# Kernel tuning notes

Hardware: AMD Instinct MI355X
Metric: run time of the kernel (lower is better)

Reference implementation:

```python
import jax, jax.numpy as jnp
import numpy as np
from jax.scipy.special import logsumexp

B, T, D, K, H, A, EH = 256, 4096, 3, 2, 2, 5, 8


def setup_inputs() -> dict:
    key = jax.random.key(0)
    ks = jax.random.split(key, 14)
    p = lambda k, shape: jax.random.normal(k, shape, jnp.float32) * 0.1
    return {
        "x": jax.random.normal(ks[0], (B, T, D), jnp.float32),
        "Q_seq": jax.random.normal(ks[1], (B, T, A, 2), jnp.float32),
        "log_pi": p(ks[2], (K,)),
        "log_A": p(ks[3], (K, K)),
        "fc1_w": p(ks[4], (EH, D)),
        "fc1_b": p(ks[5], (EH,)),
        "fc2_w": p(ks[6], (K, EH)),
        "fc2_b": p(ks[7], (K,)),
        "w_ih": p(ks[8], (3 * H, D)),
        "w_hh": p(ks[9], (3 * H, H)),
        "b_ih": p(ks[10], (3 * H,)),
        "b_hh": p(ks[11], (3 * H,)),
        "Wg": p(ks[12], (K, H, A)),
        "by": p(ks[13], (K, 2)),
    }


def reference(x, Q_seq, log_pi, log_A, fc1_w, fc1_b, fc2_w, fc2_b,
              w_ih, w_hh, b_ih, b_hh, Wg, by):
    Bn, Tn, _ = x.shape
    Hn = w_hh.shape[1]

    # ---- GRU (torch semantics: r,z,n gate order) ----
    def gru_step(h, xt):
        gi = xt @ w_ih.T + b_ih            # [B,3H]
        gh = h @ w_hh.T + b_hh
        ir, iz, inn = jnp.split(gi, 3, axis=-1)
        hr, hz, hn = jnp.split(gh, 3, axis=-1)
        r = jax.nn.sigmoid(ir + hr)
        z = jax.nn.sigmoid(iz + hz)
        n = jnp.tanh(inn + r * hn)
        h_new = (1.0 - z) * n + z * h
        return h_new, h_new

    xs = jnp.swapaxes(x, 0, 1)             # [T,B,D]
    _, hs = jax.lax.scan(gru_step, jnp.zeros((Bn, Hn), x.dtype), xs)
    h = jnp.swapaxes(hs, 0, 1)             # [B,T,H]

    # ---- Phase emitter ----
    e = jax.nn.log_softmax(jnp.tanh(x @ fc1_w.T + fc1_b) @ fc2_w.T + fc2_b, axis=-1)  # [B,T,K]

    # ---- HMM forward-backward ----
    lpi = jax.nn.log_softmax(log_pi)
    lA = jax.nn.log_softmax(log_A, axis=1)
    eT = jnp.swapaxes(e, 0, 1)             # [T,B,K]

    a0 = lpi + eT[0]
    def astep(a, et):
        an = logsumexp(a[:, :, None] + lA[None], axis=1) + et
        return an, an
    _, arest = jax.lax.scan(astep, a0, eT[1:])
    alpha = jnp.concatenate([a0[None], arest], axis=0)   # [T,B,K]

    bN = jnp.zeros_like(a0)
    def bstep(b, et1):
        bt = logsumexp(b[:, None, :] + lA[None] + et1[:, None, :], axis=2)
        return bt, bt
    _, brest = jax.lax.scan(bstep, bN, eT[1:], reverse=True)
    beta = jnp.concatenate([brest, bN[None]], axis=0)    # [T,B,K]

    lg = alpha + beta
    lg = lg - logsumexp(lg, axis=-1, keepdims=True)
    log_gamma = jnp.swapaxes(lg, 0, 1)     # [B,T,K]
    gamma = jnp.exp(log_gamma)

    # ---- Mixture-of-agents gating ----
    Wh = jnp.einsum('bth,kha->btka', h, Wg)
    gk = jax.nn.softmax(Wh, axis=-1)
    g = jnp.einsum('btk,btka->bta', gamma, gk)
    V = jnp.einsum('bta,btay->bty', g, Q_seq) + jnp.einsum('btk,kc->btc', gamma, by)
    pi_log = jax.nn.log_softmax(V, axis=-1)
    return pi_log, g, log_gamma
```

## Files before the change

### kernel.cpp

```cpp
#include <hip/hip_runtime.h>
#include <hip/hip_fp16.h>
#include <math.h>

constexpr int Bn = 256;
constexpr int Tn = 4096;
constexpr int BT = Bn * Tn;

constexpr int CG  = 32;
constexpr int CAc = 64;
constexpr int CBc = 64;
constexpr int NGRU = (Tn / CG)  * (Bn / 64);
constexpr int NALP = (Tn / CAc) * (Bn / 64);
constexpr int NBET = (Tn / CBc) * (Bn / 64);

struct __align__(8) h4 { __half2 x, y; };

typedef float  v2f __attribute__((ext_vector_type(2)));

__device__ __forceinline__ float2 f2(float a, float b){ return make_float2(a,b); }
__device__ __forceinline__ float2 f2s(float a){ return make_float2(a,a); }
__device__ __forceinline__ float2 f2mul(float2 a, float2 b){ return f2(a.x*b.x, a.y*b.y); }
__device__ __forceinline__ float2 f2fma(float2 a, float2 b, float2 c){
  return f2(fmaf(a.x,b.x,c.x), fmaf(a.y,b.y,c.y)); }

__device__ __forceinline__ __half2 h2c(float v){ return __float2half2_rn(v); }

__device__ __forceinline__ __half2 sig2h(__half2 x) {
  __half2 x2 = __hmul2(x, x);
  __half2 p = __hfma2(x2, h2c(2.0833333e-3f), h2c(-2.0833333e-2f));
  p = __hfma2(x2, p, h2c(0.25f));
  return __hfma2(x, p, h2c(0.5f));
}
__device__ __forceinline__ __half2 tanh2h(__half2 x) {
  __half2 x2 = __hmul2(x, x);
  __half2 num = __hfma2(x2, __hadd2(x2, h2c(105.f)), h2c(945.f));
  __half2 den = __hfma2(x2, __hfma2(x2, h2c(15.f), h2c(420.f)), h2c(945.f));
  float2 df = __half22float2(den);
  __half2 rd = __floats2half2_rn(__builtin_amdgcn_rcpf(df.x),
                                 __builtin_amdgcn_rcpf(df.y));
  return __hmul2(__hmul2(x, num), rd);
}

__global__ __launch_bounds__(256) void k1_pre(
    const float* __restrict__ x,
    const float* __restrict__ fc1_w, const float* __restrict__ fc1_b,
    const float* __restrict__ fc2_w, const float* __restrict__ fc2_b,
    const float* __restrict__ w_ih,  const float* __restrict__ b_ih,
    const float* __restrict__ b_hh,
    h4* __restrict__ grz, __half2* __restrict__ gn, __half2* __restrict__ E)
{
  __shared__ h4      Lg[16][17];
  __shared__ __half2 Ln[16][17];
  __shared__ __half2 LE[16][17];
  int tid = threadIdx.x;
  int btile = blockIdx.x >> 8;
  int ttile = blockIdx.x & 255;

  {
    int bl = tid >> 4, tl = tid & 15;
    int b = btile * 16 + bl, t = ttile * 16 + tl;
    const float* xp = x + ((size_t)b * Tn + t) * 3;
    float x0 = xp[0], x1 = xp[1], x2 = xp[2];

    float gr0 = fmaf(x2, w_ih[2],  fmaf(x1, w_ih[1],  fmaf(x0, w_ih[0],  b_ih[0] + b_hh[0])));
    float gr1 = fmaf(x2, w_ih[5],  fmaf(x1, w_ih[4],  fmaf(x0, w_ih[3],  b_ih[1] + b_hh[1])));
    float gz0 = fmaf(x2, w_ih[8],  fmaf(x1, w_ih[7],  fmaf(x0, w_ih[6],  b_ih[2] + b_hh[2])));
    float gz1 = fmaf(x2, w_ih[11], fmaf(x1, w_ih[10], fmaf(x0, w_ih[9],  b_ih[3] + b_hh[3])));
    float gn0 = fmaf(x2, w_ih[14], fmaf(x1, w_ih[13], fmaf(x0, w_ih[12], b_ih[4])));
    float gn1 = fmaf(x2, w_ih[17], fmaf(x1, w_ih[16], fmaf(x0, w_ih[15], b_ih[5])));

    float zk0 = fc2_b[0], zk1 = fc2_b[1];
#pragma unroll
    for (int u = 0; u < 8; ++u) {
      float a = fmaf(x2, fc1_w[u*3+2], fmaf(x1, fc1_w[u*3+1], fmaf(x0, fc1_w[u*3+0], fc1_b[u])));
      float e2 = __expf(2.0f * a);
      float th = 1.0f - 2.0f * __builtin_amdgcn_rcpf(1.0f + e2);
      zk0 = fmaf(th, fc2_w[u], zk0);
      zk1 = fmaf(th, fc2_w[8 + u], zk1);
    }
    float m = fmaxf(zk0, zk1);
    h4 g; g.x = __float22half2_rn(f2(gr0, gr1)); g.y = __float22half2_rn(f2(gz0, gz1));
    Lg[tl][bl] = g;
    Ln[tl][bl] = __float22half2_rn(f2(gn0, gn1));
    LE[tl][bl] = __float22half2_rn(f2(__expf(zk0 - m), __expf(zk1 - m)));
  }
  __syncthreads();
  {
    int tl = tid >> 4, bl = tid & 15;
    int b = btile * 16 + bl, t = ttile * 16 + tl;
    size_t o = (size_t)t * Bn + b;
    grz[o] = Lg[tl][bl];
    gn[o]  = Ln[tl][bl];
    E[o]   = LE[tl][bl];
  }
}

#define GRU_LOAD(BG, BN_, S0) \
  { _Pragma("unroll") for (int i = 0; i < 8; ++i) { \
      BG[i] = gp[(size_t)((S0) + i) * Bn]; BN_[i] = np[(size_t)((S0) + i) * Bn]; } }

#define GRU_GROUP(BG, BN_, S0, ST) \
  { _Pragma("unroll") for (int i = 0; i < 8; ++i) { \
      __half2 gA = BG[i].x, gB = BG[i].y, gN = BN_[i]; \
      __half2 h00 = __low2half2(hh), h11 = __high2half2(hh); \
      __half2 pr = __hfma2(h00, Wr0h, __hfma2(h11, Wr1h, gA)); \
      __half2 pz = __hfma2(h00, Wz0h, __hfma2(h11, Wz1h, gB)); \
      __half2 hn = __hfma2(h00, Wn0h, __hfma2(h11, Wn1h, Bnh)); \
      __half2 r = sig2h(pr), z = sig2h(pz); \
      __half2 n = tanh2h(__hfma2(r, hn, gN)); \
      hh = __hfma2(z, __hsub2(hh, n), n); \
      if (ST) hp[(size_t)((S0) + i) * Bn] = hh; \
  } }

#define ALP_LOAD(BUF, TB) \
  { _Pragma("unroll") for (int i = 0; i < 16; ++i) { BUF[i] = Ep[(size_t)((TB) + i) * Bn]; } }

#define ALP_GROUP(BUF, TB, ST, SK) \
  { _Pragma("unroll") for (int i = 0; i < 16; ++i) { \
      float2 e2 = __half22float2(BUF[i]); \
      if (!((SK) && i == 0)) { \
        av = f2mul(f2fma(f2s(av.y), A1v, f2mul(f2s(av.x), A0v)), e2); } \
      if (ST) ap[(size_t)((TB) + i) * Bn] = __float22half2_rn(av); \
      if (i == 7 || i == 15) { \
        float rs = __builtin_amdgcn_rcpf(av.x + av.y); av.x *= rs; av.y *= rs; } \
  } }

#define BET_LOAD(BUF, TB, CL) \
  { _Pragma("unroll") for (int i = 0; i < 16; ++i) { \
      int li = (TB) + 1 - i; if ((CL) && i == 0) li = Tn - 1; \
      BUF[i] = Ep[(size_t)li * Bn]; } }

#define BET_GROUP(BUF, TB, ST, SK) \
  { _Pragma("unroll") for (int i = 0; i < 16; ++i) { \
      float2 e2 = __half22float2(BUF[i]); \
      if (!((SK) && i == 0)) { \
        float2 f = f2mul(e2, bv); \
        bv = f2fma(f2s(f.y), AB1, f2mul(f2s(f.x), AB0)); } \
      if (ST) bp[(size_t)((TB) - i) * Bn] = __float22half2_rn(bv); \
      if (i == 7 || i == 15) { \
        float rs = __builtin_amdgcn_rcpf(bv.x + bv.y); bv.x *= rs; bv.y *= rs; } \
  } }

__global__ __launch_bounds__(64) void k2_scan(
    const h4* __restrict__ grz, const __half2* __restrict__ gn,
    const __half2* __restrict__ E,
    __half2* __restrict__ h, __half2* __restrict__ alpha, __half2* __restrict__ beta,
    const float* __restrict__ w_hh, const float* __restrict__ b_hh,
    const float* __restrict__ log_pi, const float* __restrict__ log_A)
{
  int blk = blockIdx.x;
  int lane = threadIdx.x;

  if (blk < NGRU) {
    int c = blk >> 2;
    int b = ((blk & 3) << 6) + lane;
    int t0 = c * CG;
    int tstart = (c >= 2) ? (t0 - 64) : 0;
    int ng = (c == 0) ? 4 : ((c == 1) ? 8 : 12);
    int wg = (c == 0) ? 0 : ((c == 1) ? 4 : 8);
    const h4*      gp = grz + (size_t)tstart * Bn + b;
    const __half2* np = gn  + (size_t)tstart * Bn + b;
    __half2*       hp = h   + (size_t)tstart * Bn + b;

    __half2 Wr0h = __floats2half2_rn(w_hh[0], w_hh[2]);
    __half2 Wr1h = __floats2half2_rn(w_hh[1], w_hh[3]);
    __half2 Wz0h = __floats2half2_rn(w_hh[4], w_hh[6]);
    __half2 Wz1h = __floats2half2_rn(w_hh[5], w_hh[7]);
    __half2 Wn0h = __floats2half2_rn(w_hh[8], w_hh[10]);
    __half2 Wn1h = __floats2half2_rn(w_hh[9], w_hh[11]);
    __half2 Bnh  = __floats2half2_rn(b_hh[4], b_hh[5]);

    __half2 hh = h2c(0.f);
    h4 AG[8], BG[8];
    __half2 AN[8], BN[8];
    GRU_LOAD(AG, AN, 0);
    GRU_LOAD(BG, BN, 8);
    for (int g = 0; g < ng; g += 2) {
      { bool st = g >= wg; GRU_GROUP(AG, AN, g * 8, st); }
      if (g + 2 < ng) GRU_LOAD(AG, AN, (g + 2) * 8);
      { bool st = (g + 1) >= wg; GRU_GROUP(BG, BN, (g + 1) * 8, st); }
      if (g + 3 < ng) GRU_LOAD(BG, BN, (g + 3) * 8);
    }
  } else if (blk < NGRU + NALP) {
    int bk = blk - NGRU;
    int c = bk >> 2;
    int b = ((bk & 3) << 6) + lane;
    int t0 = c * CAc;
    const __half2* Ep = E + b;
    __half2* ap = alpha + b;

    float la0 = log_A[0], la1 = log_A[1], la2 = log_A[2], la3 = log_A[3];
    float m0 = fmaxf(la0, la1), m1 = fmaxf(la2, la3);
    float e00 = __expf(la0 - m0), e01 = __expf(la1 - m0);
    float e10 = __expf(la2 - m1), e11 = __expf(la3 - m1);
    float i0 = 1.0f / (e00 + e01), i1 = 1.0f / (e10 + e11);
    float2 A0v = f2(e00*i0, e01*i0), A1v = f2(e10*i1, e11*i1);

    float2 av;
    int tlo, ngroups, sg;
    bool skip0;
    if (c == 0) {
      float p0 = log_pi[0], p1 = log_pi[1];
      float mp = fmaxf(p0, p1);
      float2 E0 = __half22float2(Ep[0]);
      av = f2(__expf(p0 - mp) * E0.x, __expf(p1 - mp) * E0.y);
      tlo = 0; ngroups = 4; sg = 0; skip0 = true;
    } else {
      av = f2s(1.f);
      tlo = t0 - 32; ngroups = 6; sg = 2; skip0 = false;
    }

    __half2 EA[16], EB[16];
    ALP_LOAD(EA, tlo);
    ALP_LOAD(EB, tlo + 16);
    for (int g = 0; g < ngroups; g += 2) {
      { bool st = g >= sg; bool sk = skip0 && (g == 0);
        ALP_GROUP(EA, tlo + g * 16, st, sk); }
      if (g + 2 < ngroups) ALP_LOAD(EA, tlo + (g + 2) * 16);
      { bool st = (g + 1) >= sg;
        ALP_GROUP(EB, tlo + (g + 1) * 16, st, false); }
      if (g + 3 < ngroups) ALP_LOAD(EB, tlo + (g + 3) * 16);
    }
  } else {
    int bk = blk - NGRU - NALP;
    int c = bk >> 2;
    int b = ((bk & 3) << 6) + lane;
    int t0 = c * CBc;
    int t1 = t0 + CBc - 1;
    const __half2* Ep = E + b;
    __half2* bp = beta + b;

    float la0 = log_A[0], la1 = log_A[1], la2 = log_A[2], la3 = log_A[3];
    float m0 = fmaxf(la0, la1), m1 = fmaxf(la2, la3);
    float e00 = __expf(la0 - m0), e01 = __expf(la1 - m0);
    float e10 = __expf(la2 - m1), e11 = __expf(la3 - m1);
    float i0 = 1.0f / (e00 + e01), i1 = 1.0f / (e10 + e11);
    float2 AB0 = f2(e00*i0, e10*i1), AB1 = f2(e01*i0, e11*i1);

    float2 bv = f2s(1.f);
    int thi, ngroups, sg;
    bool skip0, cl0;
    if (t1 == Tn - 1) {
      thi = t1; ngroups = 4; sg = 0; skip0 = true; cl0 = true;
    } else {
      thi = t1 + 32; ngroups = 6; sg = 2; skip0 = false; cl0 = false;
    }

    __half2 FA[16], FB[16];
    BET_LOAD(FA, thi, cl0);
    BET_LOAD(FB, thi - 16, false);
    for (int g = 0; g < ngroups; g += 2) {
      { bool st = g >= sg; bool sk = skip0 && (g == 0);
        BET_GROUP(FA, thi - g * 16, st, sk); }
      if (g + 2 < ngroups) BET_LOAD(FA, thi - (g + 2) * 16, false);
      { bool st = (g + 1) >= sg;
        BET_GROUP(FB, thi - (g + 1) * 16, st, false); }
      if (g + 3 < ngroups) BET_LOAD(FB, thi - (g + 3) * 16, false);
    }
  }
}

__global__ __launch_bounds__(256) void k3_out(
    const __half2* __restrict__ h_, const __half2* __restrict__ a_,
    const __half2* __restrict__ b_, const float* __restrict__ Q,
    const float* __restrict__ Wg, const float* __restrict__ by,
    float* __restrict__ out_pi, float* __restrict__ out_g, float* __restrict__ out_lg)
{
  __shared__ __half2 Sh[16][17], Sa[16][17], Sb[16][17];
  int tid = threadIdx.x;
  int btile = blockIdx.x >> 8;
  int ttile = blockIdx.x & 255;
  {
    int tl = tid >> 4, bl = tid & 15;
    size_t o = (size_t)(ttile * 16 + tl) * Bn + btile * 16 + bl;
    Sh[tl][bl] = h_[o]; Sa[tl][bl] = a_[o]; Sb[tl][bl] = b_[o];
  }
  __syncthreads();
  int bl = tid >> 4, tl = tid & 15;
  int b = btile * 16 + bl, t = ttile * 16 + tl;
  size_t idx = (size_t)b * Tn + t;
  float2 hv = __half22float2(Sh[tl][bl]);
  float2 av = __half22float2(Sa[tl][bl]);
  float2 bv = __half22float2(Sb[tl][bl]);

  float p0 = av.x * bv.x, p1 = av.y * bv.y;
  float invs = 1.0f / (p0 + p1);
  float gamma0 = p0 * invs, gamma1 = p1 * invs;
  float lg0 = __logf(gamma0), lg1 = __logf(gamma1);

  float wh0[5], wh1[5];
#pragma unroll
  for (int a = 0; a < 5; ++a) {
    wh0[a] = fmaf(hv.y, Wg[5 + a],  hv.x * Wg[a]);
    wh1[a] = fmaf(hv.y, Wg[15 + a], hv.x * Wg[10 + a]);
  }
  float mx0 = wh0[0], mx1 = wh1[0];
#pragma unroll
  for (int a = 1; a < 5; ++a) { mx0 = fmaxf(mx0, wh0[a]); mx1 = fmaxf(mx1, wh1[a]); }
  float ex0[5], ex1[5];
  float s0 = 0.f, s1 = 0.f;
#pragma unroll
  for (int a = 0; a < 5; ++a) {
    ex0[a] = __expf(wh0[a] - mx0); s0 += ex0[a];
    ex1[a] = __expf(wh1[a] - mx1); s1 += ex1[a];
  }
  float r0 = 1.0f / s0, r1 = 1.0f / s1;
  float c0 = gamma0 * r0, c1 = gamma1 * r1;

  const v2f* q2 = (const v2f*)(Q + idx * 10);
  v2f qv[5];
#pragma unroll
  for (int a = 0; a < 5; ++a) qv[a] = __builtin_nontemporal_load(q2 + a);

  float V0 = fmaf(gamma1, by[2], gamma0 * by[0]);
  float V1 = fmaf(gamma1, by[3], gamma0 * by[1]);
  float ga[5];
#pragma unroll
  for (int a = 0; a < 5; ++a) {
    ga[a] = fmaf(c1, ex1[a], c0 * ex0[a]);
    V0 = fmaf(ga[a], qv[a].x, V0);
    V1 = fmaf(ga[a], qv[a].y, V1);
  }
#pragma unroll
  for (int a = 0; a < 5; ++a)
    __builtin_nontemporal_store(ga[a], out_g + idx * 5 + a);

  float mv = fmaxf(V0, V1);
  float l = mv + __logf(__expf(V0 - mv) + __expf(V1 - mv));
  v2f pi_v; pi_v.x = V0 - l; pi_v.y = V1 - l;
  v2f lg_v; lg_v.x = lg0;    lg_v.y = lg1;
  __builtin_nontemporal_store(pi_v, (v2f*)out_pi + idx);
  __builtin_nontemporal_store(lg_v, (v2f*)out_lg + idx);
}

extern "C" void kernel_launch(void* const* d_in, const int* in_sizes, int n_in,
                              void* d_out, int out_size, void* d_ws, size_t ws_size,
                              hipStream_t stream) {
  const float* x      = (const float*)d_in[0];
  const float* Q      = (const float*)d_in[1];
  const float* log_pi = (const float*)d_in[2];
  const float* log_A  = (const float*)d_in[3];
  const float* fc1_w  = (const float*)d_in[4];
  const float* fc1_b  = (const float*)d_in[5];
  const float* fc2_w  = (const float*)d_in[6];
  const float* fc2_b  = (const float*)d_in[7];
  const float* w_ih   = (const float*)d_in[8];
  const float* w_hh   = (const float*)d_in[9];
  const float* b_ih   = (const float*)d_in[10];
  const float* b_hh   = (const float*)d_in[11];
  const float* Wg     = (const float*)d_in[12];
  const float* by     = (const float*)d_in[13];

  char* ws = (char*)d_ws;
  h4*      grz   = (h4*)ws;
  __half2* gn    = (__half2*)(ws + (size_t)8  * BT);
  __half2* E     = (__half2*)(ws + (size_t)12 * BT);
  __half2* h     = (__half2*)(ws + (size_t)16 * BT);
  __half2* alpha = (__half2*)(ws + (size_t)20 * BT);
  __half2* beta  = (__half2*)(ws + (size_t)24 * BT);
  float* out = (float*)d_out;

  k1_pre<<<BT / 256, 256, 0, stream>>>(x, fc1_w, fc1_b, fc2_w, fc2_b, w_ih, b_ih, b_hh, grz, gn, E);
  k2_scan<<<NGRU + NALP + NBET, 64, 0, stream>>>(grz, gn, E, h, alpha, beta, w_hh, b_hh, log_pi, log_A);
  k3_out<<<BT / 256, 256, 0, stream>>>(h, alpha, beta, Q, Wg, by,
                                       out, out + (size_t)2 * BT, out + (size_t)7 * BT);
}
```

Measured before the change: 153.2 us.

## Fuse GRU/alpha/beta scans with output stage via shared memory per chunk

Merges the scan kernel and the output kernel into one kernel. Each 192-thread block runs the GRU, forward and backward scans in three waves over the same 32-step, 64-batch chunk, keeps h/alpha/beta in LDS, then computes the outputs directly. This removes the global write and read-back of three intermediate arrays and one kernel launch. In exchange it shrinks the alpha/beta chunks from 64 to 32 steps, so proportionally more warm-up recompute is done, and the output stage now waits behind the serial scans within each block.

```diff
diff --git a/kernel.cpp b/kernel.cpp
--- a/kernel.cpp
+++ b/kernel.cpp
@@ -6,16 +6,11 @@
 constexpr int Tn = 4096;
 constexpr int BT = Bn * Tn;
 
-constexpr int CG  = 32;
-constexpr int CAc = 64;
-constexpr int CBc = 64;
-constexpr int NGRU = (Tn / CG)  * (Bn / 64);
-constexpr int NALP = (Tn / CAc) * (Bn / 64);
-constexpr int NBET = (Tn / CBc) * (Bn / 64);
+constexpr int C   = 32;
+constexpr int NF  = (Tn / C) * (Bn / 64);
 
 struct __align__(8) h4 { __half2 x, y; };
-
-typedef float  v2f __attribute__((ext_vector_type(2)));
+typedef float v2f __attribute__((ext_vector_type(2)));
 
 __device__ __forceinline__ float2 f2(float a, float b){ return make_float2(a,b); }
 __device__ __forceinline__ float2 f2s(float a){ return make_float2(a,a); }
@@ -95,11 +90,11 @@
   }
 }
 
-#define GRU_LOAD(BG, BN_, S0) \
+#define GRU_LOAD(BG, BN_, BASE) \
   { _Pragma("unroll") for (int i = 0; i < 8; ++i) { \
-      BG[i] = gp[(size_t)((S0) + i) * Bn]; BN_[i] = np[(size_t)((S0) + i) * Bn]; } }
-
-#define GRU_GROUP(BG, BN_, S0, ST) \
+      BG[i] = gp[(size_t)((BASE) + i) * Bn]; BN_[i] = np[(size_t)((BASE) + i) * Bn]; } }
+
+#define GRU_GROUP(BG, BN_, BASE, ST) \
   { _Pragma("unroll") for (int i = 0; i < 8; ++i) { \
       __half2 gA = BG[i].x, gB = BG[i].y, gN = BN_[i]; \
       __half2 h00 = __low2half2(hh), h11 = __high2half2(hh); \
@@ -109,7 +104,7 @@
       __half2 r = sig2h(pr), z = sig2h(pz); \
       __half2 n = tanh2h(__hfma2(r, hn, gN)); \
       hh = __hfma2(z, __hsub2(hh, n), n); \
-      if (ST) hp[(size_t)((S0) + i) * Bn] = hh; \
+      if (ST) Lh[(BASE) + i - t0][lane] = hh; \
   } }
 
 #define ALP_LOAD(BUF, TB) \
@@ -120,7 +115,7 @@
       float2 e2 = __half22float2(BUF[i]); \
       if (!((SK) && i == 0)) { \
         av = f2mul(f2fma(f2s(av.y), A1v, f2mul(f2s(av.x), A0v)), e2); } \
-      if (ST) ap[(size_t)((TB) + i) * Bn] = __float22half2_rn(av); \
+      if (ST) La[(TB) + i - t0][lane] = __float22half2_rn(av); \
       if (i == 7 || i == 15) { \
         float rs = __builtin_amdgcn_rcpf(av.x + av.y); av.x *= rs; av.y *= rs; } \
   } }
@@ -136,31 +131,36 @@
       if (!((SK) && i == 0)) { \
         float2 f = f2mul(e2, bv); \
         bv = f2fma(f2s(f.y), AB1, f2mul(f2s(f.x), AB0)); } \
-      if (ST) bp[(size_t)((TB) - i) * Bn] = __float22half2_rn(bv); \
+      if (ST) Lb[(TB) - i - t0][lane] = __float22half2_rn(bv); \
       if (i == 7 || i == 15) { \
         float rs = __builtin_amdgcn_rcpf(bv.x + bv.y); bv.x *= rs; bv.y *= rs; } \
   } }
 
-__global__ __launch_bounds__(64) void k2_scan(
-    const h4* __restrict__ grz, const __half2* __restrict__ gn,
+__global__ __launch_bounds__(192) void k2_fused(
+    const h4* __restrict__ grz, const __half2* __restrict__ gnp_,
     const __half2* __restrict__ E,
-    __half2* __restrict__ h, __half2* __restrict__ alpha, __half2* __restrict__ beta,
+    const float* __restrict__ Q,
     const float* __restrict__ w_hh, const float* __restrict__ b_hh,
-    const float* __restrict__ log_pi, const float* __restrict__ log_A)
+    const float* __restrict__ log_pi, const float* __restrict__ log_A,
+    const float* __restrict__ Wg, const float* __restrict__ by,
+    float* __restrict__ out_pi, float* __restrict__ out_g, float* __restrict__ out_lg)
 {
-  int blk = blockIdx.x;
-  int lane = threadIdx.x;
-
-  if (blk < NGRU) {
-    int c = blk >> 2;
-    int b = ((blk & 3) << 6) + lane;
-    int t0 = c * CG;
-    int tstart = (c >= 2) ? (t0 - 64) : 0;
-    int ng = (c == 0) ? 4 : ((c == 1) ? 8 : 12);
-    int wg = (c == 0) ? 0 : ((c == 1) ? 4 : 8);
-    const h4*      gp = grz + (size_t)tstart * Bn + b;
-    const __half2* np = gn  + (size_t)tstart * Bn + b;
-    __half2*       hp = h   + (size_t)tstart * Bn + b;
+  __shared__ __half2 Lh[C][65], La[C][65], Lb[C][65];
+
+  int tch = blockIdx.x >> 2;
+  int bq  = blockIdx.x & 3;
+  int t0  = tch * C;
+  int wave = threadIdx.x >> 6;
+  int lane = threadIdx.x & 63;
+  int b = (bq << 6) + lane;
+
+  if (wave == 0) {
+    int warm = (tch == 0) ? 0 : 32;
+    int tstart = t0 - warm;
+    int ng = (tch == 0) ? 4 : 8;
+    int wg = warm >> 3;
+    const h4*      gp = grz  + b;
+    const __half2* np = gnp_ + b;
 
     __half2 Wr0h = __floats2half2_rn(w_hh[0], w_hh[2]);
     __half2 Wr1h = __floats2half2_rn(w_hh[1], w_hh[3]);
@@ -173,21 +173,16 @@
     __half2 hh = h2c(0.f);
     h4 AG[8], BG[8];
     __half2 AN[8], BN[8];
-    GRU_LOAD(AG, AN, 0);
-    GRU_LOAD(BG, BN, 8);
+    GRU_LOAD(AG, AN, tstart);
+    GRU_LOAD(BG, BN, tstart + 8);
     for (int g = 0; g < ng; g += 2) {
-      { bool st = g >= wg; GRU_GROUP(AG, AN, g * 8, st); }
-      if (g + 2 < ng) GRU_LOAD(AG, AN, (g + 2) * 8);
-      { bool st = (g + 1) >= wg; GRU_GROUP(BG, BN, (g + 1) * 8, st); }
-      if (g + 3 < ng) GRU_LOAD(BG, BN, (g + 3) * 8);
-    }
-  } else if (blk < NGRU + NALP) {
-    int bk = blk - NGRU;
-    int c = bk >> 2;
-    int b = ((bk & 3) << 6) + lane;
-    int t0 = c * CAc;
+      { bool st = g >= wg; GRU_GROUP(AG, AN, tstart + g * 8, st); }
+      if (g + 2 < ng) GRU_LOAD(AG, AN, tstart + (g + 2) * 8);
+      { bool st = (g + 1) >= wg; GRU_GROUP(BG, BN, tstart + (g + 1) * 8, st); }
+      if (g + 3 < ng) GRU_LOAD(BG, BN, tstart + (g + 3) * 8);
+    }
+  } else if (wave == 1) {
     const __half2* Ep = E + b;
-    __half2* ap = alpha + b;
 
     float la0 = log_A[0], la1 = log_A[1], la2 = log_A[2], la3 = log_A[3];
     float m0 = fmaxf(la0, la1), m1 = fmaxf(la2, la3);
@@ -199,15 +194,15 @@
     float2 av;
     int tlo, ngroups, sg;
     bool skip0;
-    if (c == 0) {
+    if (tch == 0) {
       float p0 = log_pi[0], p1 = log_pi[1];
       float mp = fmaxf(p0, p1);
       float2 E0 = __half22float2(Ep[0]);
       av = f2(__expf(p0 - mp) * E0.x, __expf(p1 - mp) * E0.y);
-      tlo = 0; ngroups = 4; sg = 0; skip0 = true;
+      tlo = 0; ngroups = 2; sg = 0; skip0 = true;
     } else {
       av = f2s(1.f);
-      tlo = t0 - 32; ngroups = 6; sg = 2; skip0 = false;
+      tlo = t0 - 32; ngroups = 4; sg = 2; skip0 = false;
     }
 
     __half2 EA[16], EB[16];
@@ -222,13 +217,8 @@
       if (g + 3 < ngroups) ALP_LOAD(EB, tlo + (g + 3) * 16);
     }
   } else {
-    int bk = blk - NGRU - NALP;
-    int c = bk >> 2;
-    int b = ((bk & 3) << 6) + lane;
-    int t0 = c * CBc;
-    int t1 = t0 + CBc - 1;
+    int t1 = t0 + C - 1;
     const __half2* Ep = E + b;
-    __half2* bp = beta + b;
 
     float la0 = log_A[0], la1 = log_A[1], la2 = log_A[2], la3 = log_A[3];
     float m0 = fmaxf(la0, la1), m1 = fmaxf(la2, la3);
@@ -241,9 +231,9 @@
     int thi, ngroups, sg;
     bool skip0, cl0;
     if (t1 == Tn - 1) {
-      thi = t1; ngroups = 4; sg = 0; skip0 = true; cl0 = true;
+      thi = t1; ngroups = 2; sg = 0; skip0 = true; cl0 = true;
     } else {
-      thi = t1 + 32; ngroups = 6; sg = 2; skip0 = false; cl0 = false;
+      thi = t1 + 32; ngroups = 4; sg = 2; skip0 = false; cl0 = false;
     }
 
     __half2 FA[16], FB[16];
@@ -258,79 +248,77 @@
       if (g + 3 < ngroups) BET_LOAD(FB, thi - (g + 3) * 16, false);
     }
   }
-}
-
-__global__ __launch_bounds__(256) void k3_out(
-    const __half2* __restrict__ h_, const __half2* __restrict__ a_,
-    const __half2* __restrict__ b_, const float* __restrict__ Q,
-    const float* __restrict__ Wg, const float* __restrict__ by,
-    float* __restrict__ out_pi, float* __restrict__ out_g, float* __restrict__ out_lg)
-{
-  __shared__ __half2 Sh[16][17], Sa[16][17], Sb[16][17];
+
+  __syncthreads();
+
+  float wgr[20], byv[4];
+#pragma unroll
+  for (int i = 0; i < 20; ++i) wgr[i] = Wg[i];
+#pragma unroll
+  for (int i = 0; i < 4; ++i) byv[i] = by[i];
+
   int tid = threadIdx.x;
-  int btile = blockIdx.x >> 8;
-  int ttile = blockIdx.x & 255;
-  {
-    int tl = tid >> 4, bl = tid & 15;
-    size_t o = (size_t)(ttile * 16 + tl) * Bn + btile * 16 + bl;
-    Sh[tl][bl] = h_[o]; Sa[tl][bl] = a_[o]; Sb[tl][bl] = b_[o];
+#pragma unroll
+  for (int k = 0; k < 11; ++k) {
+    int e = tid + k * 192;
+    if (e < 64 * C) {
+      int bl = e >> 5, tl = e & 31;
+      int gb = (bq << 6) + bl;
+      size_t idx = (size_t)gb * Tn + (t0 + tl);
+      float2 hv = __half22float2(Lh[tl][bl]);
+      float2 av = __half22float2(La[tl][bl]);
+      float2 bv = __half22float2(Lb[tl][bl]);
+
+      float p0 = av.x * bv.x, p1 = av.y * bv.y;
+      float invs = 1.0f / (p0 + p1);
+      float gamma0 = p0 * invs, gamma1 = p1 * invs;
+      float lg0 = __logf(gamma0), lg1 = __logf(gamma1);
+
+      float wh0[5], wh1[5];
+#pragma unroll
+      for (int a = 0; a < 5; ++a) {
+        wh0[a] = fmaf(hv.y, wgr[5 + a],  hv.x * wgr[a]);
+        wh1[a] = fmaf(hv.y, wgr[15 + a], hv.x * wgr[10 + a]);
+      }
+      float mx0 = wh0[0], mx1 = wh1[0];
+#pragma unroll
+      for (int a = 1; a < 5; ++a) { mx0 = fmaxf(mx0, wh0[a]); mx1 = fmaxf(mx1, wh1[a]); }
+      float ex0[5], ex1[5];
+      float s0 = 0.f, s1 = 0.f;
+#pragma unroll
+      for (int a = 0; a < 5; ++a) {
+        ex0[a] = __expf(wh0[a] - mx0); s0 += ex0[a];
+        ex1[a] = __expf(wh1[a] - mx1); s1 += ex1[a];
+      }
+      float r0 = 1.0f / s0, r1 = 1.0f / s1;
+      float c0 = gamma0 * r0, c1 = gamma1 * r1;
+
+      const v2f* q2 = (const v2f*)(Q + idx * 10);
+      v2f qv[5];
+#pragma unroll
+      for (int a = 0; a < 5; ++a) qv[a] = __builtin_nontemporal_load(q2 + a);
+
+      float V0 = fmaf(gamma1, byv[2], gamma0 * byv[0]);
+      float V1 = fmaf(gamma1, byv[3], gamma0 * byv[1]);
+      float ga[5];
+#pragma unroll
+      for (int a = 0; a < 5; ++a) {
+        ga[a] = fmaf(c1, ex1[a], c0 * ex0[a]);
+        V0 = fmaf(ga[a], qv[a].x, V0);
+        V1 = fmaf(ga[a], qv[a].y, V1);
+      }
+#pragma unroll
+      for (int a = 0; a < 5; ++a)
+        __builtin_nontemporal_store(ga[a], out_g + idx * 5 + a);
+
+      float mv = fmaxf(V0, V1);
+      float l = mv + __logf(__expf(V0 - mv) + __expf(V1 - mv));
+      v2f pi_v; pi_v.x = V0 - l; pi_v.y = V1 - l;
+      v2f lg_v; lg_v.x = lg0;    lg_v.y = lg1;
+      __builtin_nontemporal_store(pi_v, (v2f*)out_pi + idx);
+      __builtin_nontemporal_store(lg_v, (v2f*)out_lg + idx);
+    }
   }
-  __syncthreads();
-  int bl = tid >> 4, tl = tid & 15;
-  int b = btile * 16 + bl, t = ttile * 16 + tl;
-  size_t idx = (size_t)b * Tn + t;
-  float2 hv = __half22float2(Sh[tl][bl]);
-  float2 av = __half22float2(Sa[tl][bl]);
-  float2 bv = __half22float2(Sb[tl][bl]);
-
-  float p0 = av.x * bv.x, p1 = av.y * bv.y;
-  float invs = 1.0f / (p0 + p1);
-  float gamma0 = p0 * invs, gamma1 = p1 * invs;
-  float lg0 = __logf(gamma0), lg1 = __logf(gamma1);
-
-  float wh0[5], wh1[5];
-#pragma unroll
-  for (int a = 0; a < 5; ++a) {
-    wh0[a] = fmaf(hv.y, Wg[5 + a],  hv.x * Wg[a]);
-    wh1[a] = fmaf(hv.y, Wg[15 + a], hv.x * Wg[10 + a]);
-  }
-  float mx0 = wh0[0], mx1 = wh1[0];
-#pragma unroll
-  for (int a = 1; a < 5; ++a) { mx0 = fmaxf(mx0, wh0[a]); mx1 = fmaxf(mx1, wh1[a]); }
-  float ex0[5], ex1[5];
-  float s0 = 0.f, s1 = 0.f;
-#pragma unroll
-  for (int a = 0; a < 5; ++a) {
-    ex0[a] = __expf(wh0[a] - mx0); s0 += ex0[a];
-    ex1[a] = __expf(wh1[a] - mx1); s1 += ex1[a];
-  }
-  float r0 = 1.0f / s0, r1 = 1.0f / s1;
-  float c0 = gamma0 * r0, c1 = gamma1 * r1;
-
-  const v2f* q2 = (const v2f*)(Q + idx * 10);
-  v2f qv[5];
-#pragma unroll
-  for (int a = 0; a < 5; ++a) qv[a] = __builtin_nontemporal_load(q2 + a);
-
-  float V0 = fmaf(gamma1, by[2], gamma0 * by[0]);
-  float V1 = fmaf(gamma1, by[3], gamma0 * by[1]);
-  float ga[5];
-#pragma unroll
-  for (int a = 0; a < 5; ++a) {
-    ga[a] = fmaf(c1, ex1[a], c0 * ex0[a]);
-    V0 = fmaf(ga[a], qv[a].x, V0);
-    V1 = fmaf(ga[a], qv[a].y, V1);
-  }
-#pragma unroll
-  for (int a = 0; a < 5; ++a)
-    __builtin_nontemporal_store(ga[a], out_g + idx * 5 + a);
-
-  float mv = fmaxf(V0, V1);
-  float l = mv + __logf(__expf(V0 - mv) + __expf(V1 - mv));
-  v2f pi_v; pi_v.x = V0 - l; pi_v.y = V1 - l;
-  v2f lg_v; lg_v.x = lg0;    lg_v.y = lg1;
-  __builtin_nontemporal_store(pi_v, (v2f*)out_pi + idx);
-  __builtin_nontemporal_store(lg_v, (v2f*)out_lg + idx);
 }
 
 extern "C" void kernel_launch(void* const* d_in, const int* in_sizes, int n_in,
@@ -352,16 +340,12 @@
   const float* by     = (const float*)d_in[13];
 
   char* ws = (char*)d_ws;
-  h4*      grz   = (h4*)ws;
-  __half2* gn    = (__half2*)(ws + (size_t)8  * BT);
-  __half2* E     = (__half2*)(ws + (size_t)12 * BT);
-  __half2* h     = (__half2*)(ws + (size_t)16 * BT);
-  __half2* alpha = (__half2*)(ws + (size_t)20 * BT);
-  __half2* beta  = (__half2*)(ws + (size_t)24 * BT);
+  h4*      grz = (h4*)ws;
+  __half2* gn  = (__half2*)(ws + (size_t)8  * BT);
+  __half2* E   = (__half2*)(ws + (size_t)12 * BT);
   float* out = (float*)d_out;
 
   k1_pre<<<BT / 256, 256, 0, stream>>>(x, fc1_w, fc1_b, fc2_w, fc2_b, w_ih, b_ih, b_hh, grz, gn, E);
-  k2_scan<<<NGRU + NALP + NBET, 64, 0, stream>>>(grz, gn, E, h, alpha, beta, w_hh, b_hh, log_pi, log_A);
-  k3_out<<<BT / 256, 256, 0, stream>>>(h, alpha, beta, Q, Wg, by,
-                                       out, out + (size_t)2 * BT, out + (size_t)7 * BT);
-}
+  k2_fused<<<NF, 192, 0, stream>>>(grz, gn, E, Q, w_hh, b_hh, log_pi, log_A, Wg, by,
+                                   out, out + (size_t)2 * BT, out + (size_t)7 * BT);
+}
```

Result: faster. 146.7 us (-4.2%).
